# Kernel tuning notes

Hardware: AMD Instinct MI355X
Metric: run time of the kernel (lower is better)

The kernel has to match this reference:

```python
import jax, jax.numpy as jnp
import numpy as np

B, L, HID, LAT, EXP, NL, H, D = 8, 512, 256, 256, 2, 3, 96, 8
INNER = LAT * EXP


def _layernorm(x, g, b, eps=1e-5):
    mu = x.mean(-1, keepdims=True)
    var = ((x - mu) ** 2).mean(-1, keepdims=True)
    return (x - mu) / jnp.sqrt(var + eps) * g + b


def _rmsnorm(x, w, eps=1e-6):
    return x * jax.lax.rsqrt((x * x).mean(-1, keepdims=True) + eps) * w


def _mamba_block(h, in_w, conv_w, decay, scale, out_w, rms_w):
    # h: [B, L, LAT]
    Lh = h.shape[1]
    xp = h @ in_w                      # [B, L, 2*INNER]
    u, g = jnp.split(xp, 2, axis=-1)   # each [B, L, INNER]
    # causal depthwise conv, kernel 3, left pad 2
    up = jnp.pad(u, ((0, 0), (2, 0), (0, 0)))
    uc = (conv_w[:, 0] * up[:, :Lh]
          + conv_w[:, 1] * up[:, 1:Lh + 1]
          + conv_w[:, 2] * up[:, 2:Lh + 2])
    d = jax.nn.sigmoid(decay)          # [INNER]
    inp = (1.0 - d) * scale * uc       # [B, L, INNER]
    log_d = jnp.log(jnp.clip(d, 1e-6, None))
    t = jnp.arange(Lh, dtype=h.dtype)
    diff = t[:, None] - t[None, :]     # [L, L]
    causal = (diff >= 0).astype(h.dtype)
    # M: [L, L, INNER] quadratic causal decay tensor (as in the torch code)
    M = jnp.exp(jnp.maximum(diff, 0.0)[:, :, None] * log_d) * causal[:, :, None]
    y = jnp.einsum('tkd,bkd->btd', M, inp) * jax.nn.sigmoid(g)
    return _rmsnorm(y @ out_w, rms_w)


def setup_inputs() -> dict:
    key = jax.random.key(0)
    ks = jax.random.split(key, 8)
    s = 0.02
    return {
        'x': jax.random.normal(ks[0], (B, L, HID), jnp.float32),
        'in_proj_w': jax.random.normal(ks[1], (HID, LAT), jnp.float32) * s,
        'in_ln_g': jnp.ones((LAT,), jnp.float32),
        'in_ln_b': jnp.zeros((LAT,), jnp.float32),
        'norms_g': jnp.ones((NL, LAT), jnp.float32),
        'norms_b': jnp.zeros((NL, LAT), jnp.float32),
        'blk_in_w': jax.random.normal(ks[2], (NL, LAT, 2 * INNER), jnp.float32) * s,
        'blk_conv_w': jax.random.normal(ks[3], (NL, INNER, 3), jnp.float32) * s,
        'blk_decay': jnp.zeros((NL, INNER), jnp.float32),
        'blk_scale': jnp.ones((NL, INNER), jnp.float32),
        'blk_out_w': jax.random.normal(ks[4], (NL, INNER, LAT), jnp.float32) * s,
        'blk_rms_w': jnp.ones((NL, LAT), jnp.float32),
        'head_w1': jax.random.normal(ks[5], (LAT, LAT), jnp.float32) * s,
        'head_b1': jnp.zeros((LAT,), jnp.float32),
        'head_ln_g': jnp.ones((LAT,), jnp.float32),
        'head_ln_b': jnp.zeros((LAT,), jnp.float32),
        'head_w2': jax.random.normal(ks[6], (LAT, H * D), jnp.float32) * s,
        'head_b2': jnp.zeros((H * D,), jnp.float32),
        'forecast_horizon': H,
        'input_dim': D,
    }


def reference(x, in_proj_w, in_ln_g, in_ln_b, norms_g, norms_b,
              blk_in_w, blk_conv_w, blk_decay, blk_scale, blk_out_w, blk_rms_w,
              head_w1, head_b1, head_ln_g, head_ln_b, head_w2, head_b2,
              forecast_horizon, input_dim):
    Bx = x.shape[0]
    h = _layernorm(x @ in_proj_w, in_ln_g, in_ln_b)
    for i in range(NL):
        hn = _layernorm(h, norms_g[i], norms_b[i])
        h = h + _mamba_block(hn, blk_in_w[i], blk_conv_w[i], blk_decay[i],
                             blk_scale[i], blk_out_w[i], blk_rms_w[i])
    pooled = h.mean(axis=1) * 0.5 + h[:, -1, :] * 0.5
    z = _layernorm(pooled @ head_w1 + head_b1, head_ln_g, head_ln_b)
    z = jax.nn.gelu(z, approximate=False)  # torch nn.GELU default = exact erf
    out = z @ head_w2 + head_b2            # dropout inactive at eval
    return out.reshape(Bx, forecast_horizon, input_dim)
```

## Files before the change

### kernel.cpp

```cpp
#include <hip/hip_runtime.h>
#include <math.h>


typedef __attribute__((ext_vector_type(8))) __bf16 bf16x8;
typedef __attribute__((ext_vector_type(4))) float f32x4;

__device__ __forceinline__ unsigned short f2b(float f) {
  unsigned int x = __float_as_uint(f);
  unsigned int r = (x + 0x7fffu + ((x >> 16) & 1u)) >> 16;
  return (unsigned short)r;
}
__device__ __forceinline__ float b2f(unsigned short u) {
  return __uint_as_float(((unsigned int)u) << 16);
}

__device__ __forceinline__ void wave_reduce2(float& a, float& b) {
#pragma unroll
  for (int off = 32; off > 0; off >>= 1) {
    a += __shfl_xor(a, off, 64);
    b += __shfl_xor(b, off, 64);
  }
}
__device__ __forceinline__ float wave_reduce1(float a) {
#pragma unroll
  for (int off = 32; off > 0; off >>= 1) a += __shfl_xor(a, off, 64);
  return a;
}

#define GLD16(gsrc, ldst)                                              \
  __builtin_amdgcn_global_load_lds(                                    \
      (const __attribute__((address_space(1))) void*)(gsrc),           \
      (__attribute__((address_space(3))) void*)(ldst), 16, 0, 0)

__global__ __launch_bounds__(256) void k_setup(
    const float* __restrict__ inproj, const float* __restrict__ binw,
    const float* __restrict__ boutw, const float* __restrict__ x,
    unsigned short* __restrict__ inwT, unsigned short* __restrict__ binwT,
    unsigned short* __restrict__ boutwT, unsigned short* __restrict__ xb) {
  const int z = blockIdx.z;
  if (z == 7) {
    const int q = blockIdx.y * 32 + blockIdx.x;
#pragma unroll
    for (int j = 0; j < 2; ++j) {
      int i = q * 512 + threadIdx.x + j * 256;
      float4 v = ((const float4*)x)[i];
      ushort4 o;
      o.x = f2b(v.x); o.y = f2b(v.y); o.z = f2b(v.z); o.w = f2b(v.w);
      ((ushort4*)xb)[i] = o;
    }
    return;
  }
  __shared__ float t[32][33];
  const float* src;
  unsigned short* dst;
  int R, Cc;
  if (z == 0) {
    src = inproj; dst = inwT; R = 256; Cc = 256;
  } else if (z <= 3) {
    src = binw + (size_t)(z - 1) * 256 * 1024;
    dst = binwT + (size_t)(z - 1) * 1024 * 256;
    R = 256; Cc = 1024;
  } else {
    src = boutw + (size_t)(z - 4) * 512 * 256;
    dst = boutwT + (size_t)(z - 4) * 256 * 512;
    R = 512; Cc = 256;
  }
  const int bx = blockIdx.x, by = blockIdx.y;
  if (bx * 32 >= Cc || by * 32 >= R) return;
  const int tx = threadIdx.x & 31, ty = threadIdx.x >> 5;
#pragma unroll
  for (int j = 0; j < 4; ++j)
    t[ty + j * 8][tx] = src[(size_t)(by * 32 + ty + j * 8) * Cc + bx * 32 + tx];
  __syncthreads();
#pragma unroll
  for (int j = 0; j < 4; ++j)
    dst[(size_t)(bx * 32 + ty + j * 8) * R + by * 32 + tx] = f2b(t[tx][ty + j * 8]);
}

__global__ __launch_bounds__(256) void k_gemm2_scan(
    const unsigned short* __restrict__ A,
    const unsigned short* __restrict__ Bt,
    const float* __restrict__ cw, const float* __restrict__ decay,
    const float* __restrict__ scl, unsigned short* __restrict__ y) {
  __shared__ unsigned short sA[2][512 * 32];
  __shared__ unsigned short sB[2][32 * 32];
  __shared__ float su[16 * 520];
  __shared__ float sg[16 * 520];
  __shared__ float lend[16][16];
  __shared__ float carry[16][16];
  const int b = blockIdx.y;
  const int d0 = blockIdx.x * 16;
  const int tid = threadIdx.x;
  const int lane = tid & 63;
  const int w = tid >> 6;
  const int fr = lane & 15, fg = lane >> 4;
  const unsigned short* Ab = A + (size_t)b * 512 * 256;

#define STAGE2(buf, kt)                                                     \
  {                                                                         \
    for (int j = 0; j < 8; ++j) {                                           \
      int idx = tid + j * 256;                                              \
      int row = idx >> 2, slot = idx & 3;                                   \
      GLD16(Ab + (size_t)row * 256 + (kt) + slot * 8, &sA[buf][idx * 8]);   \
    }                                                                       \
    if (tid < 128) {                                                        \
      int row = tid >> 2, slot = tid & 3;                                   \
      int gr = row < 16 ? d0 + row : 496 + d0 + row;                        \
      GLD16(Bt + (size_t)gr * 256 + (kt) + slot * 8, &sB[buf][tid * 8]);    \
    }                                                                       \
  }

  f32x4 au[8] = {}, ag[8] = {};
  STAGE2(0, 0);
  __syncthreads();
#pragma unroll
  for (int ph = 0; ph < 8; ++ph) {
    const int cur = ph & 1;
    if (ph < 7) STAGE2(cur ^ 1, (ph + 1) * 32);
    bf16x8 bu = *(const bf16x8*)&sB[cur][fr * 32 + fg * 8];
    bf16x8 bg = *(const bf16x8*)&sB[cur][(16 + fr) * 32 + fg * 8];
#pragma unroll
    for (int m = 0; m < 8; ++m) {
      bf16x8 af = *(const bf16x8*)&sA[cur][(w * 128 + m * 16 + fr) * 32 + fg * 8];
      au[m] = __builtin_amdgcn_mfma_f32_16x16x32_bf16(af, bu, au[m], 0, 0, 0);
      ag[m] = __builtin_amdgcn_mfma_f32_16x16x32_bf16(af, bg, ag[m], 0, 0, 0);
    }
    __syncthreads();
  }
#undef STAGE2
#pragma unroll
  for (int m = 0; m < 8; ++m)
#pragma unroll
    for (int j = 0; j < 4; ++j) {
      int row = w * 128 + m * 16 + fg * 4 + j;
      int off = (row >> 5) * 520 + (row & 31) * 16 + fr;
      su[off] = au[m][j];
      sg[off] = ag[m][j];
    }
  __syncthreads();
  const int ds = tid & 15, ch = tid >> 4;
  const int d = d0 + ds;
  const float a = 1.f / (1.f + __expf(-decay[d]));
  const float coef = (1.f - a) * scl[d];
  const float cw0 = cw[d * 3], cw1 = cw[d * 3 + 1], cw2 = cw[d * 3 + 2];
  const int T0 = ch * 32;
  float um1 = T0 >= 1 ? su[((T0 - 1) >> 5) * 520 + ((T0 - 1) & 31) * 16 + ds] : 0.f;
  float um2 = T0 >= 2 ? su[((T0 - 2) >> 5) * 520 + ((T0 - 2) & 31) * 16 + ds] : 0.f;
  float s = 0.f, s0r[32];
#pragma unroll
  for (int t = 0; t < 32; ++t) {
    float u = su[ch * 520 + t * 16 + ds];
    float uc = fmaf(cw0, um2, fmaf(cw1, um1, cw2 * u));
    s = fmaf(a, s, coef * uc);
    s0r[t] = s;
    um2 = um1;
    um1 = u;
  }
  lend[ch][ds] = s;
  __syncthreads();
  if (tid < 16) {
    float aa = 1.f / (1.f + __expf(-decay[d0 + tid]));
    float a32 = aa * aa;
    a32 = a32 * a32;
    a32 = a32 * a32;
    a32 = a32 * a32;
    a32 = a32 * a32;
    float c = 0.f;
#pragma unroll
    for (int j = 0; j < 16; ++j) {
      carry[j][tid] = c;
      c = fmaf(a32, c, lend[j][tid]);
    }
  }
  __syncthreads();
  const float c = carry[ch][ds];
  unsigned short* yp = y + ((size_t)b * 512 + T0) * 512 + d;
  float ap = a;
#pragma unroll
  for (int t = 0; t < 32; ++t) {
    float gv = sg[ch * 520 + t * 16 + ds];
    float sv = fmaf(ap, c, s0r[t]);
    float sig = 1.f / (1.f + __expf(-gv));
    yp[(size_t)t * 512] = f2b(sv * sig);
    ap *= a;
  }
}

template <int KTOT, int MODE>
__global__ __launch_bounds__(256) void k_gemm_epi(
    const unsigned short* __restrict__ A, const unsigned short* __restrict__ Bt,
    const float* __restrict__ p1, const float* __restrict__ p2,
    const float* __restrict__ g2, const float* __restrict__ b2,
    float* __restrict__ h, unsigned short* __restrict__ hnb,
    float* __restrict__ part) {
  constexpr int NP = KTOT / 32;
  __shared__ __align__(16) unsigned char smem[(2 * (16 * 32 + 256 * 32)) * 2];
  __shared__ float ppart[4][256];
  unsigned short* sA0 = (unsigned short*)smem;
  unsigned short* sB0 = sA0 + 2 * 16 * 32;
  float* ep = (float*)smem;
  const int tid = threadIdx.x;
  const int lane = tid & 63;
  const int wc = tid >> 6;
  const int bm0 = blockIdx.x * 16;
  const int fr = lane & 15, fg = lane >> 4;

#define STAGEE(buf, kt)                                                     \
  {                                                                         \
    if (tid < 64) {                                                         \
      int row = tid >> 2, slot = tid & 3;                                   \
      GLD16(A + (size_t)(bm0 + row) * KTOT + (kt) + slot * 8,               \
            &sA0[(buf) * 512 + tid * 8]);                                   \
    }                                                                       \
    for (int j = 0; j < 4; ++j) {                                           \
      int idx = tid + j * 256;                                              \
      int row = idx >> 2, slot = idx & 3;                                   \
      GLD16(Bt + (size_t)row * KTOT + (kt) + slot * 8,                      \
            &sB0[(buf) * 8192 + idx * 8]);                                  \
    }                                                                       \
  }

  f32x4 acc[4] = {};
  STAGEE(0, 0);
  __syncthreads();
#pragma unroll
  for (int ph = 0; ph < NP; ++ph) {
    const int cur = ph & 1;
    if (ph < NP - 1) STAGEE(cur ^ 1, (ph + 1) * 32);
    bf16x8 af = *(const bf16x8*)&sA0[cur * 512 + fr * 32 + fg * 8];
    bf16x8 bf[4];
#pragma unroll
    for (int n = 0; n < 4; ++n)
      bf[n] = *(const bf16x8*)&sB0[cur * 8192 + (wc * 64 + n * 16 + fr) * 32 + fg * 8];
#pragma unroll
    for (int n = 0; n < 4; ++n)
      acc[n] = __builtin_amdgcn_mfma_f32_16x16x32_bf16(af, bf[n], acc[n], 0, 0, 0);
    __syncthreads();
  }
#undef STAGEE
#pragma unroll
  for (int n = 0; n < 4; ++n)
#pragma unroll
    for (int j = 0; j < 4; ++j)
      ep[(fg * 4 + j) * 260 + wc * 64 + n * 16 + fr] = acc[n][j];
  __syncthreads();
  const int c0 = lane * 4;
  float4 q1 = *(const float4*)&p1[c0];
  float4 q2v = (MODE == 0) ? *(const float4*)&p2[c0] : float4{0, 0, 0, 0};
  float4 gg2 = (MODE != 2) ? *(const float4*)&g2[c0] : float4{0, 0, 0, 0};
  float4 bb2 = (MODE != 2) ? *(const float4*)&b2[c0] : float4{0, 0, 0, 0};
  float4 psum = {0.f, 0.f, 0.f, 0.f};
#pragma unroll
  for (int r = 0; r < 4; ++r) {
    const int row = wc * 4 + r;
    const size_t grow = (size_t)(bm0 + row) * 256 + c0;
    float4 v = *(const float4*)&ep[row * 260 + c0];
    float4 hh;
    if (MODE == 0) {
      float s = v.x + v.y + v.z + v.w;
      float sq = v.x * v.x + v.y * v.y + v.z * v.z + v.w * v.w;
      wave_reduce2(s, sq);
      float mu = s * (1.f / 256.f);
      float rstd = rsqrtf(sq * (1.f / 256.f) - mu * mu + 1e-5f);
      hh.x = (v.x - mu) * rstd * q1.x + q2v.x;
      hh.y = (v.y - mu) * rstd * q1.y + q2v.y;
      hh.z = (v.z - mu) * rstd * q1.z + q2v.z;
      hh.w = (v.w - mu) * rstd * q1.w + q2v.w;
      *(float4*)&h[grow] = hh;
    } else {
      float sq = v.x * v.x + v.y * v.y + v.z * v.z + v.w * v.w;
      sq = wave_reduce1(sq);
      float rstd = rsqrtf(sq * (1.f / 256.f) + 1e-6f);
      hh = *(const float4*)&h[grow];
      hh.x += v.x * rstd * q1.x;
      hh.y += v.y * rstd * q1.y;
      hh.z += v.z * rstd * q1.z;
      hh.w += v.w * rstd * q1.w;
      *(float4*)&h[grow] = hh;
    }
    if (MODE != 2) {
      float s2 = hh.x + hh.y + hh.z + hh.w;
      float sq2 = hh.x * hh.x + hh.y * hh.y + hh.z * hh.z + hh.w * hh.w;
      wave_reduce2(s2, sq2);
      float mu2 = s2 * (1.f / 256.f);
      float rs2 = rsqrtf(sq2 * (1.f / 256.f) - mu2 * mu2 + 1e-5f);
      ushort4 u;
      u.x = f2b((hh.x - mu2) * rs2 * gg2.x + bb2.x);
      u.y = f2b((hh.y - mu2) * rs2 * gg2.y + bb2.y);
      u.z = f2b((hh.z - mu2) * rs2 * gg2.z + bb2.z);
      u.w = f2b((hh.w - mu2) * rs2 * gg2.w + bb2.w);
      *(ushort4*)&hnb[grow] = u;
    } else {
      psum.x += hh.x;
      psum.y += hh.y;
      psum.z += hh.z;
      psum.w += hh.w;
    }
  }
  if (MODE == 2) {
    *(float4*)&ppart[wc][c0] = psum;
    __syncthreads();
    float pv = ppart[0][tid] + ppart[1][tid] + ppart[2][tid] + ppart[3][tid];
    part[(size_t)blockIdx.x * 256 + tid] = pv;
  }
}

__global__ __launch_bounds__(1024) void k_head(
    const float* __restrict__ part, const float* __restrict__ h,
    const float* __restrict__ w1, const float* __restrict__ b1,
    const float* __restrict__ lng, const float* __restrict__ lnb,
    const float* __restrict__ w2, const float* __restrict__ b2,
    float* __restrict__ out) {
  const int b = blockIdx.x;
  const int t = threadIdx.x;
  const int ks = threadIdx.y;
  __shared__ float sp[256];
  __shared__ float sz[256];
  __shared__ float part4[4][256];
  __shared__ float red[8];
  if (ks == 0) {
    float s = 0.f;
#pragma unroll
    for (int j = 0; j < 32; ++j) s += part[((size_t)b * 32 + j) * 256 + t];
    sp[t] = s * (0.5f / 512.f) + 0.5f * h[(((size_t)b * 512) + 511) * 256 + t];
  }
  __syncthreads();
  float acc = 0.f;
#pragma unroll 8
  for (int k = ks * 64; k < ks * 64 + 64; ++k) acc += sp[k] * w1[(size_t)k * 256 + t];
  part4[ks][t] = acc;
  __syncthreads();
  if (ks == 0) {
    float aval = part4[0][t] + part4[1][t] + part4[2][t] + part4[3][t] + b1[t];
    float s = aval, sq = aval * aval;
    wave_reduce2(s, sq);
    const int lane = t & 63, w = t >> 6;
    if (lane == 0) {
      red[w] = s;
      red[4 + w] = sq;
    }
    part4[0][t] = aval;
  }
  __syncthreads();
  if (ks == 0) {
    float S = red[0] + red[1] + red[2] + red[3];
    float SQ = red[4] + red[5] + red[6] + red[7];
    float mu = S * (1.f / 256.f);
    float rstd = rsqrtf(SQ * (1.f / 256.f) - mu * mu + 1e-5f);
    float zv = (part4[0][t] - mu) * rstd * lng[t] + lnb[t];
    zv = 0.5f * zv * (1.f + erff(zv * 0.70710678118654752f));
    sz[t] = zv;
  }
  __syncthreads();
  const int col = ks * 256 + t;
  if (col < 768) {
    float a = b2[col];
#pragma unroll 8
    for (int k = 0; k < 256; ++k) a += sz[k] * w2[(size_t)k * 768 + col];
    out[(size_t)b * 768 + col] = a;
  }
}

extern "C" void kernel_launch(void* const* d_in, const int* in_sizes, int n_in,
                              void* d_out, int out_size, void* d_ws, size_t ws_size,
                              hipStream_t stream) {
  const float* x = (const float*)d_in[0];
  const float* in_proj_w = (const float*)d_in[1];
  const float* in_ln_g = (const float*)d_in[2];
  const float* in_ln_b = (const float*)d_in[3];
  const float* norms_g = (const float*)d_in[4];
  const float* norms_b = (const float*)d_in[5];
  const float* blk_in_w = (const float*)d_in[6];
  const float* blk_conv_w = (const float*)d_in[7];
  const float* blk_decay = (const float*)d_in[8];
  const float* blk_scale = (const float*)d_in[9];
  const float* blk_out_w = (const float*)d_in[10];
  const float* blk_rms_w = (const float*)d_in[11];
  const float* head_w1 = (const float*)d_in[12];
  const float* head_b1 = (const float*)d_in[13];
  const float* head_ln_g = (const float*)d_in[14];
  const float* head_ln_b = (const float*)d_in[15];
  const float* head_w2 = (const float*)d_in[16];
  const float* head_b2 = (const float*)d_in[17];

  char* wsb = (char*)d_ws;
  float* h = (float*)(wsb + 0);
  float* part = (float*)(wsb + (4 << 20));
  unsigned short* hnb = (unsigned short*)(wsb + (8 << 20));
  unsigned short* xb = (unsigned short*)(wsb + (10 << 20));
  unsigned short* yb = (unsigned short*)(wsb + (12 << 20));
  unsigned short* inwT = (unsigned short*)(wsb + (25 << 20));
  unsigned short* binwT = inwT + 65536;
  unsigned short* boutwT = binwT + 786432;
  float* out = (float*)d_out;

  k_setup<<<dim3(32, 16, 8), 256, 0, stream>>>(in_proj_w, blk_in_w, blk_out_w, x,
                                               inwT, binwT, boutwT, xb);
  k_gemm_epi<256, 0><<<256, 256, 0, stream>>>(xb, inwT, in_ln_g, in_ln_b, norms_g,
                                              norms_b, h, hnb, nullptr);
  for (int i = 0; i < 3; ++i) {
    k_gemm2_scan<<<dim3(32, 8), 256, 0, stream>>>(
        hnb, binwT + (size_t)i * 262144, blk_conv_w + i * 1536, blk_decay + i * 512,
        blk_scale + i * 512, yb);
    if (i < 2)
      k_gemm_epi<512, 1><<<256, 256, 0, stream>>>(
          yb, boutwT + (size_t)i * 131072, blk_rms_w + i * 256, nullptr,
          norms_g + (i + 1) * 256, norms_b + (i + 1) * 256, h, hnb, nullptr);
    else
      k_gemm_epi<512, 2><<<256, 256, 0, stream>>>(
          yb, boutwT + (size_t)i * 131072, blk_rms_w + i * 256, nullptr, nullptr,
          nullptr, h, nullptr, part);
  }
  k_head<<<8, dim3(256, 4), 0, stream>>>(part, h, head_w1, head_b1, head_ln_g,
                                         head_ln_b, head_w2, head_b2, out);
}
```

Baseline: 112.9 us.

## Use larger XOR-swizzled K chunks in GEMMs and fuse x bf16 conversion into first GEMM

Both GEMM kernels now stage much larger K chunks (128 for the epilogue GEMM, 64 for the scan GEMM, with the whole B slice loaded once) into an XOR-swizzled LDS layout. This cuts the number of barriers and avoids LDS bank conflicts. The first GEMM reads fp32 x directly and converts it to bf16 while loading fragments, which removes the separate x conversion pass in setup. The cost is much larger LDS footprints (about 130KB+ per block), which may limit occupancy to one block per CU.

```diff
diff --git a/kernel.cpp b/kernel.cpp
--- a/kernel.cpp
+++ b/kernel.cpp
@@ -27,6 +27,13 @@
   return a;
 }
 
+__device__ __forceinline__ bf16x8 cvt8(float4 a, float4 b) {
+  bf16x8 r;
+  r[0] = (__bf16)a.x; r[1] = (__bf16)a.y; r[2] = (__bf16)a.z; r[3] = (__bf16)a.w;
+  r[4] = (__bf16)b.x; r[5] = (__bf16)b.y; r[6] = (__bf16)b.z; r[7] = (__bf16)b.w;
+  return r;
+}
+
 #define GLD16(gsrc, ldst)                                              \
   __builtin_amdgcn_global_load_lds(                                    \
       (const __attribute__((address_space(1))) void*)(gsrc),           \
@@ -34,23 +41,10 @@
 
 __global__ __launch_bounds__(256) void k_setup(
     const float* __restrict__ inproj, const float* __restrict__ binw,
-    const float* __restrict__ boutw, const float* __restrict__ x,
-    unsigned short* __restrict__ inwT, unsigned short* __restrict__ binwT,
-    unsigned short* __restrict__ boutwT, unsigned short* __restrict__ xb) {
+    const float* __restrict__ boutw, unsigned short* __restrict__ inwT,
+    unsigned short* __restrict__ binwT, unsigned short* __restrict__ boutwT) {
+  __shared__ float t[32][33];
   const int z = blockIdx.z;
-  if (z == 7) {
-    const int q = blockIdx.y * 32 + blockIdx.x;
-#pragma unroll
-    for (int j = 0; j < 2; ++j) {
-      int i = q * 512 + threadIdx.x + j * 256;
-      float4 v = ((const float4*)x)[i];
-      ushort4 o;
-      o.x = f2b(v.x); o.y = f2b(v.y); o.z = f2b(v.z); o.w = f2b(v.w);
-      ((ushort4*)xb)[i] = o;
-    }
-    return;
-  }
-  __shared__ float t[32][33];
   const float* src;
   unsigned short* dst;
   int R, Cc;
@@ -77,167 +71,82 @@
     dst[(size_t)(bx * 32 + ty + j * 8) * R + by * 32 + tx] = f2b(t[tx][ty + j * 8]);
 }
 
-__global__ __launch_bounds__(256) void k_gemm2_scan(
-    const unsigned short* __restrict__ A,
-    const unsigned short* __restrict__ Bt,
-    const float* __restrict__ cw, const float* __restrict__ decay,
-    const float* __restrict__ scl, unsigned short* __restrict__ y) {
-  __shared__ unsigned short sA[2][512 * 32];
-  __shared__ unsigned short sB[2][32 * 32];
-  __shared__ float su[16 * 520];
-  __shared__ float sg[16 * 520];
-  __shared__ float lend[16][16];
-  __shared__ float carry[16][16];
-  const int b = blockIdx.y;
-  const int d0 = blockIdx.x * 16;
-  const int tid = threadIdx.x;
-  const int lane = tid & 63;
-  const int w = tid >> 6;
-  const int fr = lane & 15, fg = lane >> 4;
-  const unsigned short* Ab = A + (size_t)b * 512 * 256;
-
-#define STAGE2(buf, kt)                                                     \
-  {                                                                         \
-    for (int j = 0; j < 8; ++j) {                                           \
-      int idx = tid + j * 256;                                              \
-      int row = idx >> 2, slot = idx & 3;                                   \
-      GLD16(Ab + (size_t)row * 256 + (kt) + slot * 8, &sA[buf][idx * 8]);   \
-    }                                                                       \
-    if (tid < 128) {                                                        \
-      int row = tid >> 2, slot = tid & 3;                                   \
-      int gr = row < 16 ? d0 + row : 496 + d0 + row;                        \
-      GLD16(Bt + (size_t)gr * 256 + (kt) + slot * 8, &sB[buf][tid * 8]);    \
-    }                                                                       \
-  }
-
-  f32x4 au[8] = {}, ag[8] = {};
-  STAGE2(0, 0);
-  __syncthreads();
-#pragma unroll
-  for (int ph = 0; ph < 8; ++ph) {
-    const int cur = ph & 1;
-    if (ph < 7) STAGE2(cur ^ 1, (ph + 1) * 32);
-    bf16x8 bu = *(const bf16x8*)&sB[cur][fr * 32 + fg * 8];
-    bf16x8 bg = *(const bf16x8*)&sB[cur][(16 + fr) * 32 + fg * 8];
-#pragma unroll
-    for (int m = 0; m < 8; ++m) {
-      bf16x8 af = *(const bf16x8*)&sA[cur][(w * 128 + m * 16 + fr) * 32 + fg * 8];
-      au[m] = __builtin_amdgcn_mfma_f32_16x16x32_bf16(af, bu, au[m], 0, 0, 0);
-      ag[m] = __builtin_amdgcn_mfma_f32_16x16x32_bf16(af, bg, ag[m], 0, 0, 0);
-    }
-    __syncthreads();
-  }
-#undef STAGE2
-#pragma unroll
-  for (int m = 0; m < 8; ++m)
-#pragma unroll
-    for (int j = 0; j < 4; ++j) {
-      int row = w * 128 + m * 16 + fg * 4 + j;
-      int off = (row >> 5) * 520 + (row & 31) * 16 + fr;
-      su[off] = au[m][j];
-      sg[off] = ag[m][j];
-    }
-  __syncthreads();
-  const int ds = tid & 15, ch = tid >> 4;
-  const int d = d0 + ds;
-  const float a = 1.f / (1.f + __expf(-decay[d]));
-  const float coef = (1.f - a) * scl[d];
-  const float cw0 = cw[d * 3], cw1 = cw[d * 3 + 1], cw2 = cw[d * 3 + 2];
-  const int T0 = ch * 32;
-  float um1 = T0 >= 1 ? su[((T0 - 1) >> 5) * 520 + ((T0 - 1) & 31) * 16 + ds] : 0.f;
-  float um2 = T0 >= 2 ? su[((T0 - 2) >> 5) * 520 + ((T0 - 2) & 31) * 16 + ds] : 0.f;
-  float s = 0.f, s0r[32];
-#pragma unroll
-  for (int t = 0; t < 32; ++t) {
-    float u = su[ch * 520 + t * 16 + ds];
-    float uc = fmaf(cw0, um2, fmaf(cw1, um1, cw2 * u));
-    s = fmaf(a, s, coef * uc);
-    s0r[t] = s;
-    um2 = um1;
-    um1 = u;
-  }
-  lend[ch][ds] = s;
-  __syncthreads();
-  if (tid < 16) {
-    float aa = 1.f / (1.f + __expf(-decay[d0 + tid]));
-    float a32 = aa * aa;
-    a32 = a32 * a32;
-    a32 = a32 * a32;
-    a32 = a32 * a32;
-    a32 = a32 * a32;
-    float c = 0.f;
-#pragma unroll
-    for (int j = 0; j < 16; ++j) {
-      carry[j][tid] = c;
-      c = fmaf(a32, c, lend[j][tid]);
-    }
-  }
-  __syncthreads();
-  const float c = carry[ch][ds];
-  unsigned short* yp = y + ((size_t)b * 512 + T0) * 512 + d;
-  float ap = a;
-#pragma unroll
-  for (int t = 0; t < 32; ++t) {
-    float gv = sg[ch * 520 + t * 16 + ds];
-    float sv = fmaf(ap, c, s0r[t]);
-    float sig = 1.f / (1.f + __expf(-gv));
-    yp[(size_t)t * 512] = f2b(sv * sig);
-    ap *= a;
-  }
-}
-
-template <int KTOT, int MODE>
+template <int KTOT, int MODE, bool AF32>
 __global__ __launch_bounds__(256) void k_gemm_epi(
-    const unsigned short* __restrict__ A, const unsigned short* __restrict__ Bt,
+    const void* __restrict__ A, const unsigned short* __restrict__ Bt,
     const float* __restrict__ p1, const float* __restrict__ p2,
     const float* __restrict__ g2, const float* __restrict__ b2,
     float* __restrict__ h, unsigned short* __restrict__ hnb,
     float* __restrict__ part) {
-  constexpr int NP = KTOT / 32;
-  __shared__ __align__(16) unsigned char smem[(2 * (16 * 32 + 256 * 32)) * 2];
+  constexpr int NCH = KTOT / 128;
+  constexpr int ABYTES = AF32 ? 8192 : 4096;
+  __shared__ __align__(16) unsigned char smem[2 * ABYTES + 2 * 65536];
   __shared__ float ppart[4][256];
-  unsigned short* sA0 = (unsigned short*)smem;
-  unsigned short* sB0 = sA0 + 2 * 16 * 32;
+  unsigned char* sAb = smem;
+  unsigned char* sBb = smem + 2 * ABYTES;
   float* ep = (float*)smem;
+  const float* Af = (const float*)A;
+  const unsigned short* Ab = (const unsigned short*)A;
   const int tid = threadIdx.x;
   const int lane = tid & 63;
   const int wc = tid >> 6;
   const int bm0 = blockIdx.x * 16;
   const int fr = lane & 15, fg = lane >> 4;
 
-#define STAGEE(buf, kt)                                                     \
-  {                                                                         \
-    if (tid < 64) {                                                         \
-      int row = tid >> 2, slot = tid & 3;                                   \
-      GLD16(A + (size_t)(bm0 + row) * KTOT + (kt) + slot * 8,               \
-            &sA0[(buf) * 512 + tid * 8]);                                   \
-    }                                                                       \
-    for (int j = 0; j < 4; ++j) {                                           \
-      int idx = tid + j * 256;                                              \
-      int row = idx >> 2, slot = idx & 3;                                   \
-      GLD16(Bt + (size_t)row * KTOT + (kt) + slot * 8,                      \
-            &sB0[(buf) * 8192 + idx * 8]);                                  \
-    }                                                                       \
-  }
+  auto stage = [&](int buf, int c) {
+    if (AF32) {
+#pragma unroll
+      for (int j = 0; j < 2; ++j) {
+        int idx = tid + j * 256;
+        int row = idx >> 5, p = idx & 31, l = p ^ (row & 7);
+        GLD16(Af + (size_t)(bm0 + row) * KTOT + c * 128 + l * 4,
+              sAb + buf * ABYTES + idx * 16);
+      }
+    } else {
+      int row = tid >> 4, p = tid & 15, l = p ^ (row & 7);
+      GLD16(Ab + (size_t)(bm0 + row) * KTOT + c * 128 + l * 8,
+            sAb + buf * ABYTES + tid * 16);
+    }
+#pragma unroll
+    for (int j = 0; j < 16; ++j) {
+      int idx = tid + j * 256;
+      int row = idx >> 4, p = idx & 15, l = p ^ (row & 7);
+      GLD16(Bt + (size_t)row * KTOT + c * 128 + l * 8, sBb + buf * 65536 + idx * 16);
+    }
+  };
 
   f32x4 acc[4] = {};
-  STAGEE(0, 0);
-  __syncthreads();
-#pragma unroll
-  for (int ph = 0; ph < NP; ++ph) {
-    const int cur = ph & 1;
-    if (ph < NP - 1) STAGEE(cur ^ 1, (ph + 1) * 32);
-    bf16x8 af = *(const bf16x8*)&sA0[cur * 512 + fr * 32 + fg * 8];
-    bf16x8 bf[4];
-#pragma unroll
-    for (int n = 0; n < 4; ++n)
-      bf[n] = *(const bf16x8*)&sB0[cur * 8192 + (wc * 64 + n * 16 + fr) * 32 + fg * 8];
-#pragma unroll
-    for (int n = 0; n < 4; ++n)
-      acc[n] = __builtin_amdgcn_mfma_f32_16x16x32_bf16(af, bf[n], acc[n], 0, 0, 0);
+  stage(0, 0);
+  for (int c = 0; c < NCH; ++c) {
+    const int cur = c & 1;
     __syncthreads();
-  }
-#undef STAGEE
+    if (c + 1 < NCH) stage(cur ^ 1, c + 1);
+#pragma unroll
+    for (int kk = 0; kk < 128; kk += 32) {
+      bf16x8 af;
+      if (AF32) {
+        int l0 = (kk >> 2) + fg * 2;
+        int p0 = l0 ^ (fr & 7), p1 = (l0 + 1) ^ (fr & 7);
+        const float* base = (const float*)(sAb + cur * ABYTES) + fr * 128;
+        float4 v0 = *(const float4*)(base + p0 * 4);
+        float4 v1 = *(const float4*)(base + p1 * 4);
+        af = cvt8(v0, v1);
+      } else {
+        int p = ((kk >> 3) + fg) ^ (fr & 7);
+        af = *(const bf16x8*)((const unsigned short*)(sAb + cur * ABYTES) + fr * 128 +
+                              p * 8);
+      }
+      int pb = ((kk >> 3) + fg) ^ (fr & 7);
+#pragma unroll
+      for (int n = 0; n < 4; ++n) {
+        const unsigned short* bp = (const unsigned short*)(sBb + cur * 65536) +
+                                   (wc * 64 + n * 16 + fr) * 128 + pb * 8;
+        acc[n] = __builtin_amdgcn_mfma_f32_16x16x32_bf16(af, *(const bf16x8*)bp,
+                                                         acc[n], 0, 0, 0);
+      }
+    }
+  }
+  __syncthreads();
 #pragma unroll
   for (int n = 0; n < 4; ++n)
 #pragma unroll
@@ -305,6 +214,126 @@
   }
 }
 
+__global__ __launch_bounds__(256) void k_gemm2_scan(
+    const unsigned short* __restrict__ A,
+    const unsigned short* __restrict__ Bt,
+    const float* __restrict__ cw, const float* __restrict__ decay,
+    const float* __restrict__ scl, unsigned short* __restrict__ y) {
+  __shared__ __align__(16) unsigned char smem[16384 + 2 * 65536];
+  unsigned short* sB = (unsigned short*)smem;
+  unsigned char* qb = smem + 16384;
+  float* su = (float*)(smem + 16384);
+  float* sg = su + 8320;
+  float* lend = sg + 8320;
+  float* carry = lend + 256;
+  const int b = blockIdx.y;
+  const int d0 = blockIdx.x * 16;
+  const int tid = threadIdx.x;
+  const int lane = tid & 63;
+  const int w = tid >> 6;
+  const int fr = lane & 15, fg = lane >> 4;
+  const unsigned short* Abp = A + (size_t)b * 512 * 256;
+
+  auto stageQ = [&](int buf, int q) {
+#pragma unroll
+    for (int j = 0; j < 16; ++j) {
+      int idx = tid + j * 256;
+      int row = idx >> 3, p = idx & 7, l = p ^ (row & 7);
+      GLD16(Abp + (size_t)row * 256 + q * 64 + l * 8, qb + buf * 65536 + idx * 16);
+    }
+  };
+#pragma unroll
+  for (int j = 0; j < 4; ++j) {
+    int idx = tid + j * 256;
+    int row = idx >> 5, p = idx & 31, l = p ^ (row & 7);
+    int gr = row < 16 ? d0 + row : 496 + d0 + row;
+    GLD16(Bt + (size_t)gr * 256 + l * 8, smem + idx * 16);
+  }
+  stageQ(0, 0);
+
+  f32x4 au[8] = {}, ag[8] = {};
+#pragma unroll
+  for (int q = 0; q < 4; ++q) {
+    const int cq = q & 1;
+    __syncthreads();
+    if (q < 3) stageQ(cq ^ 1, q + 1);
+#pragma unroll
+    for (int kk = 0; kk < 64; kk += 32) {
+      int lb = q * 8 + (kk >> 3) + fg;
+      int pb = lb ^ (fr & 7);
+      bf16x8 bu = *(const bf16x8*)&sB[fr * 256 + pb * 8];
+      bf16x8 bg = *(const bf16x8*)&sB[(16 + fr) * 256 + pb * 8];
+      int pa = ((kk >> 3) + fg) ^ (fr & 7);
+#pragma unroll
+      for (int m = 0; m < 8; ++m) {
+        int row = w * 128 + m * 16 + fr;
+        bf16x8 af =
+            *(const bf16x8*)((const unsigned short*)(qb + cq * 65536) + row * 64 +
+                             pa * 8);
+        au[m] = __builtin_amdgcn_mfma_f32_16x16x32_bf16(af, bu, au[m], 0, 0, 0);
+        ag[m] = __builtin_amdgcn_mfma_f32_16x16x32_bf16(af, bg, ag[m], 0, 0, 0);
+      }
+    }
+  }
+  __syncthreads();
+#pragma unroll
+  for (int m = 0; m < 8; ++m)
+#pragma unroll
+    for (int j = 0; j < 4; ++j) {
+      int row = w * 128 + m * 16 + fg * 4 + j;
+      int off = (row >> 5) * 520 + (row & 31) * 16 + fr;
+      su[off] = au[m][j];
+      sg[off] = ag[m][j];
+    }
+  __syncthreads();
+  const int ds = tid & 15, ch = tid >> 4;
+  const int d = d0 + ds;
+  const float a = 1.f / (1.f + __expf(-decay[d]));
+  const float coef = (1.f - a) * scl[d];
+  const float cw0 = cw[d * 3], cw1 = cw[d * 3 + 1], cw2 = cw[d * 3 + 2];
+  const int T0 = ch * 32;
+  float um1 = T0 >= 1 ? su[((T0 - 1) >> 5) * 520 + ((T0 - 1) & 31) * 16 + ds] : 0.f;
+  float um2 = T0 >= 2 ? su[((T0 - 2) >> 5) * 520 + ((T0 - 2) & 31) * 16 + ds] : 0.f;
+  float s = 0.f, s0r[32];
+#pragma unroll
+  for (int t = 0; t < 32; ++t) {
+    float u = su[ch * 520 + t * 16 + ds];
+    float uc = fmaf(cw0, um2, fmaf(cw1, um1, cw2 * u));
+    s = fmaf(a, s, coef * uc);
+    s0r[t] = s;
+    um2 = um1;
+    um1 = u;
+  }
+  lend[ch * 16 + ds] = s;
+  __syncthreads();
+  if (tid < 16) {
+    float aa = 1.f / (1.f + __expf(-decay[d0 + tid]));
+    float a32 = aa * aa;
+    a32 = a32 * a32;
+    a32 = a32 * a32;
+    a32 = a32 * a32;
+    a32 = a32 * a32;
+    float c = 0.f;
+#pragma unroll
+    for (int j = 0; j < 16; ++j) {
+      carry[j * 16 + tid] = c;
+      c = fmaf(a32, c, lend[j * 16 + tid]);
+    }
+  }
+  __syncthreads();
+  const float c = carry[ch * 16 + ds];
+  unsigned short* yp = y + ((size_t)b * 512 + T0) * 512 + d;
+  float ap = a;
+#pragma unroll
+  for (int t = 0; t < 32; ++t) {
+    float gv = sg[ch * 520 + t * 16 + ds];
+    float sv = fmaf(ap, c, s0r[t]);
+    float sig = 1.f / (1.f + __expf(-gv));
+    yp[(size_t)t * 512] = f2b(sv * sig);
+    ap *= a;
+  }
+}
+
 __global__ __launch_bounds__(1024) void k_head(
     const float* __restrict__ part, const float* __restrict__ h,
     const float* __restrict__ w1, const float* __restrict__ b1,
@@ -387,27 +416,26 @@
   float* h = (float*)(wsb + 0);
   float* part = (float*)(wsb + (4 << 20));
   unsigned short* hnb = (unsigned short*)(wsb + (8 << 20));
-  unsigned short* xb = (unsigned short*)(wsb + (10 << 20));
   unsigned short* yb = (unsigned short*)(wsb + (12 << 20));
   unsigned short* inwT = (unsigned short*)(wsb + (25 << 20));
   unsigned short* binwT = inwT + 65536;
   unsigned short* boutwT = binwT + 786432;
   float* out = (float*)d_out;
 
-  k_setup<<<dim3(32, 16, 8), 256, 0, stream>>>(in_proj_w, blk_in_w, blk_out_w, x,
-                                               inwT, binwT, boutwT, xb);
-  k_gemm_epi<256, 0><<<256, 256, 0, stream>>>(xb, inwT, in_ln_g, in_ln_b, norms_g,
-                                              norms_b, h, hnb, nullptr);
+  k_setup<<<dim3(32, 16, 7), 256, 0, stream>>>(in_proj_w, blk_in_w, blk_out_w, inwT,
+                                               binwT, boutwT);
+  k_gemm_epi<256, 0, true><<<256, 256, 0, stream>>>(
+      x, inwT, in_ln_g, in_ln_b, norms_g, norms_b, h, hnb, nullptr);
   for (int i = 0; i < 3; ++i) {
     k_gemm2_scan<<<dim3(32, 8), 256, 0, stream>>>(
         hnb, binwT + (size_t)i * 262144, blk_conv_w + i * 1536, blk_decay + i * 512,
         blk_scale + i * 512, yb);
     if (i < 2)
-      k_gemm_epi<512, 1><<<256, 256, 0, stream>>>(
+      k_gemm_epi<512, 1, false><<<256, 256, 0, stream>>>(
           yb, boutwT + (size_t)i * 131072, blk_rms_w + i * 256, nullptr,
           norms_g + (i + 1) * 256, norms_b + (i + 1) * 256, h, hnb, nullptr);
     else
-      k_gemm_epi<512, 2><<<256, 256, 0, stream>>>(
+      k_gemm_epi<512, 2, false><<<256, 256, 0, stream>>>(
           yb, boutwT + (size_t)i * 131072, blk_rms_w + i * 256, nullptr, nullptr,
           nullptr, h, nullptr, part);
   }
```

Measured after the change: 98.30 us. -12.9%, faster.
